# Optimization experiments

Hardware: AMD Instinct MI355X
Metric: run time of the kernel (lower is better)

## Reference

```python
import jax, jax.numpy as jnp
import numpy as np

H, KV, D, EPS = 32, 8, 128, 1e-6
G = H // KV  # kv groups = 4
ROPE_THETA = 5000000.0


def _rms_norm(x, gamma):
    # x: (..., D)
    return x * jax.lax.rsqrt(jnp.mean(x * x, axis=-1, keepdims=True) + EPS) * gamma


def _rotate_half(x):
    x1, x2 = jnp.split(x, 2, axis=-1)
    return jnp.concatenate([-x2, x1], axis=-1)


def _apply_rope(x, cos, sin):
    # x: (b, h, s, D); cos/sin: (b, s, 1, D) -> (b, 1, s, D)
    cos = jnp.transpose(cos, (0, 2, 1, 3))
    sin = jnp.transpose(sin, (0, 2, 1, 3))
    return x * cos + _rotate_half(x) * sin


def setup_inputs() -> dict:
    key = jax.random.key(0)
    ks = jax.random.split(key, 8)
    b, s, hid = 2, 2048, 2560
    hidden = jax.random.normal(ks[0], (b, s, hid), dtype=jnp.float32)
    # realistic RoPE tables (half-split convention matching _rotate_half)
    inv_freq = 1.0 / (ROPE_THETA ** (np.arange(0, D, 2, dtype=np.float32) / D))  # (D/2,)
    pos = np.arange(s, dtype=np.float32)
    freqs = np.outer(pos, inv_freq)                     # (s, D/2)
    emb = np.concatenate([freqs, freqs], axis=-1)       # (s, D)
    cos = jnp.broadcast_to(jnp.asarray(np.cos(emb))[None, :, None, :], (b, s, 1, D))
    sin = jnp.broadcast_to(jnp.asarray(np.sin(emb))[None, :, None, :], (b, s, 1, D))
    sc = 1.0 / np.sqrt(hid)
    wq = jax.random.normal(ks[1], (H * D, hid), dtype=jnp.float32) * sc
    wk = jax.random.normal(ks[2], (KV * D, hid), dtype=jnp.float32) * sc
    wv = jax.random.normal(ks[3], (KV * D, hid), dtype=jnp.float32) * sc
    wo = jax.random.normal(ks[4], (hid, H * D), dtype=jnp.float32) * (1.0 / np.sqrt(H * D))
    q_gamma = jnp.ones((D,), dtype=jnp.float32)
    k_gamma = jnp.ones((D,), dtype=jnp.float32)
    return {"hidden": hidden, "cos": cos, "sin": sin, "wq": wq, "wk": wk,
            "wv": wv, "wo": wo, "q_gamma": q_gamma, "k_gamma": k_gamma}


def reference(hidden, cos, sin, wq, wk, wv, wo, q_gamma, k_gamma):
    b, s, _ = hidden.shape
    # projections -> (b, heads, s, D)
    q = (hidden @ wq.T).reshape(b, s, H, D).transpose(0, 2, 1, 3)
    k = (hidden @ wk.T).reshape(b, s, KV, D).transpose(0, 2, 1, 3)
    v = (hidden @ wv.T).reshape(b, s, KV, D).transpose(0, 2, 1, 3)
    # QK-RMSNorm over head_dim
    q = _rms_norm(q, q_gamma)
    k = _rms_norm(k, k_gamma)
    # RoPE
    q = _apply_rope(q, cos, sin)
    k = _apply_rope(k, cos, sin)
    new_k, new_v = k, v  # kv cache (no prior cache)
    # GQA attention without materializing expanded K/V
    qg = q.reshape(b, KV, G, s, D)
    scale = 1.0 / np.sqrt(D)
    scores = jnp.einsum('bkgqd,bkld->bkgql', qg, k) * scale  # (b,KV,G,s,s)
    causal = jnp.tril(jnp.ones((s, s), dtype=bool))
    scores = jnp.where(causal, scores, jnp.finfo(scores.dtype).min)
    probs = jax.nn.softmax(scores, axis=-1)
    out = jnp.einsum('bkgql,bkld->bkgqd', probs, v)          # (b,KV,G,s,D)
    out = out.reshape(b, H, s, D).transpose(0, 2, 1, 3).reshape(b, s, H * D)
    return (out @ wo.T, new_k, new_v)
```

## Files before the change

kernel.cpp:

```cpp
#include <hip/hip_runtime.h>
#include <stdint.h>

typedef unsigned short u16;
typedef __attribute__((ext_vector_type(8))) short short8;
typedef __attribute__((ext_vector_type(4))) float f32x4;

#define MFMA_BF16(a,b,c) __builtin_amdgcn_mfma_f32_16x16x32_bf16((a),(b),(c),0,0,0)

__device__ __forceinline__ u16 f2bf(float x) {
    uint32_t u = __builtin_bit_cast(uint32_t, x);
    u += 0x7fffu + ((u >> 16) & 1u);
    return (u16)(u >> 16);
}
__device__ __forceinline__ float bf2f(u16 u) {
    return __builtin_bit_cast(float, (uint32_t)u << 16);
}
__device__ __forceinline__ void glds16(const void* g, void* lds) {
    __builtin_amdgcn_global_load_lds((const __attribute__((address_space(1))) void*)g,
                                     (__attribute__((address_space(3))) void*)lds,
                                     16, 0, 0);
}

__device__ __forceinline__ void cvt4(const float* __restrict__ s,
                                     u16* __restrict__ d, int i) {
    float4 v = *(const float4*)(s + i);
    ushort4 o;
    o.x = f2bf(v.x); o.y = f2bf(v.y); o.z = f2bf(v.z); o.w = f2bf(v.w);
    *(ushort4*)(d + i) = o;
}
__global__ __launch_bounds__(256) void cvt_all(
        const float* __restrict__ s0, u16* __restrict__ d0,
        const float* __restrict__ s1, u16* __restrict__ d1,
        const float* __restrict__ s2, u16* __restrict__ d2,
        const float* __restrict__ s3, u16* __restrict__ d3,
        const float* __restrict__ s4, u16* __restrict__ d4)
{
    int i = (blockIdx.x * 256 + threadIdx.x) * 4;
    if      (i < 10485760) cvt4(s0, d0, i);
    else if (i < 20971520) cvt4(s1, d1, i - 10485760);
    else if (i < 23592960) cvt4(s2, d2, i - 20971520);
    else if (i < 26214400) cvt4(s3, d3, i - 23592960);
    else if (i < 36700160) cvt4(s4, d4, i - 26214400);
}

template<bool BF16_OUT>
__global__ __launch_bounds__(256) void gemm_bt(const u16* __restrict__ A,
                                               const u16* __restrict__ B,
                                               void* __restrict__ Cv,
                                               int K, int lda, int ldb, int ldc)
{
    __shared__ __align__(16) u16 As[128 * 64];
    __shared__ __align__(16) u16 Bs[128 * 64];
    const int t = threadIdx.x;
    const int w = t >> 6, l = t & 63;
    const int m0 = blockIdx.y * 128, n0 = blockIdx.x * 128;
    const int wm = (w & 1) * 64, wn = (w >> 1) * 64;
    const int lrow = l & 15, lk = l >> 4;

    f32x4 acc[4][4];
#pragma unroll
    for (int i = 0; i < 4; i++)
#pragma unroll
        for (int j = 0; j < 4; j++) acc[i][j] = (f32x4){0.f, 0.f, 0.f, 0.f};

    const int row_b = w * 8 + (l >> 3);
    const int gsw = ((l & 7) ^ (l >> 3)) * 8;
    const u16* Ap[4]; const u16* Bp[4];
#pragma unroll
    for (int i = 0; i < 4; i++) {
        Ap[i] = A + (size_t)(m0 + row_b + i * 32) * lda + gsw;
        Bp[i] = B + (size_t)(n0 + row_b + i * 32) * ldb + gsw;
    }
    char* Asb = (char*)As + w * 1024;
    char* Bsb = (char*)Bs + w * 1024;

    for (int k0 = 0; k0 < K; k0 += 64) {
        __syncthreads();
#pragma unroll
        for (int i = 0; i < 4; i++) glds16(Ap[i] + k0, Asb + i * 4096);
#pragma unroll
        for (int i = 0; i < 4; i++) glds16(Bp[i] + k0, Bsb + i * 4096);
        __syncthreads();
#pragma unroll
        for (int k2 = 0; k2 < 2; k2++) {
            const int slb = (k2 * 4 + lk) ^ (lrow & 7);
            short8 af[4], bf[4];
#pragma unroll
            for (int mi = 0; mi < 4; mi++)
                af[mi] = *(const short8*)&As[(wm + mi * 16 + lrow) * 64 + slb * 8];
#pragma unroll
            for (int ni = 0; ni < 4; ni++)
                bf[ni] = *(const short8*)&Bs[(wn + ni * 16 + lrow) * 64 + slb * 8];
#pragma unroll
            for (int mi = 0; mi < 4; mi++)
#pragma unroll
                for (int ni = 0; ni < 4; ni++)
                    acc[mi][ni] = MFMA_BF16(af[mi], bf[ni], acc[mi][ni]);
        }
    }

#pragma unroll
    for (int mi = 0; mi < 4; mi++) {
#pragma unroll
        for (int r = 0; r < 4; r++) {
            int row = m0 + wm + mi * 16 + lk * 4 + r;
#pragma unroll
            for (int ni = 0; ni < 4; ni++) {
                int col = n0 + wn + ni * 16 + lrow;
                float v = acc[mi][ni][r];
                if (BF16_OUT) ((u16*)Cv)[(size_t)row * ldc + col] = f2bf(v);
                else          ((float*)Cv)[(size_t)row * ldc + col] = v;
            }
        }
    }
}

__global__ __launch_bounds__(256) void norm_rope_qk(const u16* __restrict__ qkv,
        const float* __restrict__ cosb, const float* __restrict__ sinb,
        const float* __restrict__ qg, const float* __restrict__ kg,
        u16* __restrict__ qb, u16* __restrict__ kb, float* __restrict__ k_out)
{
    const int idx = blockIdx.x * 4 + (threadIdx.x >> 6);
    const int l = threadIdx.x & 63;
    const int tok = idx / 40, hd = idx - tok * 40;
    const int b = tok >> 11, pos = tok & 2047;
    const u16* row = qkv + (size_t)tok * 6144 + hd * 128;
    float x1 = bf2f(row[l]), x2 = bf2f(row[l + 64]);
    float ss = x1 * x1 + x2 * x2;
#pragma unroll
    for (int m = 1; m < 64; m <<= 1) ss += __shfl_xor(ss, m, 64);
    float rn = rsqrtf(ss * (1.0f / 128.0f) + 1e-6f);

    const float* gm = (hd < 32) ? qg : kg;
    float xn1 = x1 * rn * gm[l];
    float xn2 = x2 * rn * gm[l + 64];
    float c1 = cosb[(size_t)tok * 128 + l],      s1 = sinb[(size_t)tok * 128 + l];
    float c2 = cosb[(size_t)tok * 128 + l + 64], s2 = sinb[(size_t)tok * 128 + l + 64];
    float y1 = xn1 * c1 - xn2 * s1;
    float y2 = xn2 * c2 + xn1 * s2;
    if (hd < 32) {
        const float qs = 0.08838834764831845f;
        size_t base = (((size_t)b * 32 + hd) * 2048 + pos) * 128;
        qb[base + l]      = f2bf(y1 * qs);
        qb[base + l + 64] = f2bf(y2 * qs);
    } else {
        int kv = hd - 32;
        size_t base = (((size_t)b * 8 + kv) * 2048 + pos) * 128;
        k_out[base + l] = y1; k_out[base + l + 64] = y2;
        kb[base + l] = f2bf(y1); kb[base + l + 64] = f2bf(y2);
    }
}

__global__ __launch_bounds__(256) void v_pack(const u16* __restrict__ qkv,
        float* __restrict__ v_out, u16* __restrict__ vtb)
{
    __shared__ __align__(16) u16 T[64 * 128];
    const int pb = blockIdx.x, bkv = blockIdx.y;
    const int b = bkv >> 3, kv = bkv & 7;
    const int p0 = pb * 64;
    const int t = threadIdx.x;
    const int pos = t >> 2, ch4 = t & 3;
    const u16* src = qkv + (size_t)(b * 2048 + p0 + pos) * 6144 + (40 + kv) * 128 + ch4 * 32;
    float* vdst = v_out + ((size_t)bkv * 2048 + p0 + pos) * 128 + ch4 * 32;
#pragma unroll
    for (int j = 0; j < 4; j++) {
        short8 x = *(const short8*)(src + j * 8);
        float4 f0, f1;
        f0.x = bf2f(x[0]); f0.y = bf2f(x[1]); f0.z = bf2f(x[2]); f0.w = bf2f(x[3]);
        f1.x = bf2f(x[4]); f1.y = bf2f(x[5]); f1.z = bf2f(x[6]); f1.w = bf2f(x[7]);
        *(float4*)(vdst + j * 8)     = f0;
        *(float4*)(vdst + j * 8 + 4) = f1;
        int slot = (ch4 * 4 + j) ^ (pos & 7);
        *(short8*)&T[pos * 128 + slot * 8] = x;
    }
    __syncthreads();
    const int d = t & 127, ph = t >> 7;
    u16* obase = vtb + ((size_t)bkv * 128 + d) * 2048 + p0 + ph * 32;
#pragma unroll
    for (int g = 0; g < 4; g++) {
        short8 tv;
#pragma unroll
        for (int jj = 0; jj < 8; jj++) {
            int pp = ph * 32 + g * 8 + jj;
            int slot = (d >> 3) ^ (pp & 7);
            tv[jj] = (short)T[pp * 128 + slot * 8 + (d & 7)];
        }
        *(short8*)(obase + g * 8) = tv;
    }
}

__global__ __launch_bounds__(256, 3) void attn_kernel(const u16* __restrict__ qb,
        const u16* __restrict__ kb, const u16* __restrict__ vtb,
        u16* __restrict__ ao)
{
    __shared__ __align__(16) u16 Ks[64 * 128];
    __shared__ __align__(16) u16 Vs[128 * 64];
    __shared__ __align__(16) u16 Ps[4][32 * 72];

    const int bh = blockIdx.x;
    const int b = bh >> 5, h = bh & 31;
    const int kvh = h >> 2;
    const int qt = (int)gridDim.y - 1 - (int)blockIdx.y;
    const int q0 = qt * 128;
    const int t = threadIdx.x, w = t >> 6, l = t & 63;
    const int lrow = l & 15, lk = l >> 4;

    const u16* qbase  = qb  + ((size_t)b * 32 + h)  * 2048 * 128;
    const u16* kbase  = kb  + ((size_t)b * 8 + kvh) * 2048 * 128;
    const u16* vtbase = vtb + ((size_t)b * 8 + kvh) * 128 * 2048;

    short8 qf[2][4];
#pragma unroll
    for (int m = 0; m < 2; m++) {
        const u16* qrow = qbase + (size_t)(q0 + w * 32 + m * 16 + lrow) * 128 + lk * 8;
#pragma unroll
        for (int ks = 0; ks < 4; ks++) qf[m][ks] = *(const short8*)(qrow + ks * 32);
    }

    f32x4 o[2][8];
#pragma unroll
    for (int m = 0; m < 2; m++)
#pragma unroll
        for (int i = 0; i < 8; i++) o[m][i] = (f32x4){0.f, 0.f, 0.f, 0.f};
    float lsum[2][4] = {{0.f,0.f,0.f,0.f},{0.f,0.f,0.f,0.f}};

    int kR[4], kG[4], vR[4], vG[4];
#pragma unroll
    for (int i = 0; i < 4; i++) {
        int c = i * 256 + t;
        kR[i] = c >> 4; kG[i] = (c & 15) ^ (kR[i] & 7);
        vR[i] = c >> 3; vG[i] = (c & 7)  ^ (vR[i] & 7);
    }
    char* Ksb = (char*)Ks + w * 1024;
    char* Vsb = (char*)Vs + w * 1024;
    u16* pw = &Ps[w][0];
    const int wrow_max = q0 + w * 32 + 31;

    const int nkt = 2 * qt + 2;
    for (int kt = 0; kt < nkt; kt++) {
        const int kv0 = kt * 64;
        __syncthreads();
#pragma unroll
        for (int i = 0; i < 4; i++)
            glds16(kbase + (size_t)(kv0 + kR[i]) * 128 + kG[i] * 8, Ksb + i * 4096);
#pragma unroll
        for (int i = 0; i < 4; i++)
            glds16(vtbase + (size_t)vR[i] * 2048 + kv0 + vG[i] * 8, Vsb + i * 4096);
        __syncthreads();

        if (kv0 > wrow_max) continue;

        f32x4 s[2][4];
#pragma unroll
        for (int m = 0; m < 2; m++)
#pragma unroll
            for (int i = 0; i < 4; i++) s[m][i] = (f32x4){0.f, 0.f, 0.f, 0.f};
#pragma unroll
        for (int ks = 0; ks < 4; ks++) {
#pragma unroll
            for (int nt = 0; nt < 4; nt++) {
                int r = nt * 16 + lrow;
                int sl = (ks * 4 + lk) ^ (r & 7);
                short8 kf = *(const short8*)&Ks[r * 128 + sl * 8];
                s[0][nt] = MFMA_BF16(qf[0][ks], kf, s[0][nt]);
                s[1][nt] = MFMA_BF16(qf[1][ks], kf, s[1][nt]);
            }
        }

#pragma unroll
        for (int m = 0; m < 2; m++) {
            const int rowbase = q0 + w * 32 + m * 16;
            if (kv0 + 63 > rowbase) {
#pragma unroll
                for (int nt = 0; nt < 4; nt++) {
                    int cg = kv0 + nt * 16 + lrow;
#pragma unroll
                    for (int r = 0; r < 4; r++)
                        if (cg > rowbase + lk * 4 + r) s[m][nt][r] = -1e30f;
                }
            }
#pragma unroll
            for (int nt = 0; nt < 4; nt++)
#pragma unroll
                for (int r = 0; r < 4; r++) {
                    float p = __expf(s[m][nt][r]);
                    s[m][nt][r] = p;
                    lsum[m][r] += p;
                    pw[(m * 16 + lk * 4 + r) * 72 + nt * 16 + lrow] = f2bf(p);
                }
        }
        asm volatile("s_waitcnt lgkmcnt(0)" ::: "memory");

#pragma unroll
        for (int k2 = 0; k2 < 2; k2++) {
            short8 pf0 = *(const short8*)&pw[lrow * 72 + k2 * 32 + lk * 8];
            short8 pf1 = *(const short8*)&pw[(16 + lrow) * 72 + k2 * 32 + lk * 8];
#pragma unroll
            for (int nt = 0; nt < 8; nt++) {
                int rr = nt * 16 + lrow;
                int sl = (k2 * 4 + lk) ^ (rr & 7);
                short8 vf = *(const short8*)&Vs[rr * 64 + sl * 8];
                o[0][nt] = MFMA_BF16(pf0, vf, o[0][nt]);
                o[1][nt] = MFMA_BF16(pf1, vf, o[1][nt]);
            }
        }
    }

#pragma unroll
    for (int m = 0; m < 2; m++)
#pragma unroll
        for (int r = 0; r < 4; r++) {
            float v = lsum[m][r];
            v += __shfl_xor(v, 1, 64);
            v += __shfl_xor(v, 2, 64);
            v += __shfl_xor(v, 4, 64);
            v += __shfl_xor(v, 8, 64);
            lsum[m][r] = 1.0f / v;
        }
#pragma unroll
    for (int m = 0; m < 2; m++)
#pragma unroll
        for (int nt = 0; nt < 8; nt++)
#pragma unroll
            for (int r = 0; r < 4; r++) {
                int tok = q0 + w * 32 + m * 16 + lk * 4 + r;
                size_t off = ((size_t)b * 2048 + tok) * 4096 + h * 128 + nt * 16 + lrow;
                ao[off] = f2bf(o[m][nt][r] * lsum[m][r]);
            }
}

extern "C" void kernel_launch(void* const* d_in, const int* in_sizes, int n_in,
                              void* d_out, int out_size, void* d_ws, size_t ws_size,
                              hipStream_t stream)
{
    (void)in_sizes; (void)n_in; (void)out_size; (void)ws_size;
    const float* hidden = (const float*)d_in[0];
    const float* cosb   = (const float*)d_in[1];
    const float* sinb   = (const float*)d_in[2];
    const float* wq     = (const float*)d_in[3];
    const float* wk     = (const float*)d_in[4];
    const float* wv     = (const float*)d_in[5];
    const float* wo     = (const float*)d_in[6];
    const float* qg     = (const float*)d_in[7];
    const float* kg     = (const float*)d_in[8];

    float* out   = (float*)d_out;
    float* k_out = out + (size_t)2 * 2048 * 2560;
    float* v_out = k_out + (size_t)2 * 8 * 2048 * 128;

    u16* hid_b = (u16*)d_ws;
    u16* w_b   = hid_b + 10485760;
    u16* wo_b  = w_b   + 15728640;
    u16* q_b   = wo_b  + 10485760;
    u16* k_b   = q_b   + 16777216;
    u16* vt_b  = k_b   + 4194304;
    u16* qkv_b = vt_b  + 4194304;
    u16* ao_b  = hid_b;

    cvt_all<<<35840, 256, 0, stream>>>(hidden, hid_b, wq, w_b,
                                       wk, w_b + 10485760, wv, w_b + 13107200,
                                       wo, wo_b);

    gemm_bt<true><<<dim3(48, 32), 256, 0, stream>>>(hid_b, w_b, qkv_b,
                                                    2560, 2560, 2560, 6144);
    norm_rope_qk<<<40960, 256, 0, stream>>>(qkv_b, cosb, sinb, qg, kg,
                                            q_b, k_b, k_out);
    v_pack<<<dim3(32, 16), 256, 0, stream>>>(qkv_b, v_out, vt_b);
    attn_kernel<<<dim3(64, 16), 256, 0, stream>>>(q_b, k_b, vt_b, ao_b);
    gemm_bt<false><<<dim3(20, 32), 256, 0, stream>>>(ao_b, wo_b, out,
                                                     4096, 4096, 4096, 2560);
}
```

Baseline: 676.8 us.

## Replace GEMM with 256x256 8-wave double-buffered pipelined kernel

After: 603.9 us. -10.8%, faster.

```diff
diff --git a/kernel.cpp b/kernel.cpp
--- a/kernel.cpp
+++ b/kernel.cpp
@@ -6,6 +6,10 @@
 typedef __attribute__((ext_vector_type(4))) float f32x4;
 
 #define MFMA_BF16(a,b,c) __builtin_amdgcn_mfma_f32_16x16x32_bf16((a),(b),(c),0,0,0)
+
+#define S_BARRIER()  asm volatile("s_barrier" ::: "memory")
+#define WAIT_LGKM0() asm volatile("s_waitcnt lgkmcnt(0)" ::: "memory")
+#define WAIT_VM(N)   asm volatile("s_waitcnt vmcnt(" #N ")" ::: "memory")
 
 __device__ __forceinline__ u16 f2bf(float x) {
     uint32_t u = __builtin_bit_cast(uint32_t, x);
@@ -43,71 +47,144 @@
     else if (i < 36700160) cvt4(s4, d4, i - 26214400);
 }
 
+template<int MH, int NH>
+__device__ __forceinline__ void mm16(f32x4 (&acc)[8][4],
+                                     const short8 (&a)[4][2],
+                                     const short8 (&b)[2][2]) {
+#pragma unroll
+    for (int k2 = 0; k2 < 2; k2++)
+#pragma unroll
+        for (int mi = 0; mi < 4; mi++)
+#pragma unroll
+            for (int nj = 0; nj < 2; nj++)
+                acc[MH * 4 + mi][NH * 2 + nj] =
+                    MFMA_BF16(a[mi][k2], b[nj][k2], acc[MH * 4 + mi][NH * 2 + nj]);
+}
+
 template<bool BF16_OUT>
-__global__ __launch_bounds__(256) void gemm_bt(const u16* __restrict__ A,
-                                               const u16* __restrict__ B,
-                                               void* __restrict__ Cv,
-                                               int K, int lda, int ldb, int ldc)
-{
-    __shared__ __align__(16) u16 As[128 * 64];
-    __shared__ __align__(16) u16 Bs[128 * 64];
+__global__ __launch_bounds__(512, 2) void gemm8(const u16* __restrict__ A,
+                                                const u16* __restrict__ B,
+                                                void* __restrict__ Cv,
+                                                int K, int lda, int ldb, int ldc,
+                                                int ntn)
+{
+    __shared__ __align__(16) u16 Sm[65536];
     const int t = threadIdx.x;
     const int w = t >> 6, l = t & 63;
-    const int m0 = blockIdx.y * 128, n0 = blockIdx.x * 128;
-    const int wm = (w & 1) * 64, wn = (w >> 1) * 64;
     const int lrow = l & 15, lk = l >> 4;
-
-    f32x4 acc[4][4];
-#pragma unroll
-    for (int i = 0; i < 4; i++)
+    const int wm = w >> 2, wn = w & 3;
+
+    const int nwg = (int)gridDim.x;
+    const int cpx = nwg >> 3;
+    const int id = (int)blockIdx.x;
+    const int sw = (id & 7) * cpx + (id >> 3);
+    const int tm = sw / ntn, tn = sw - tm * ntn;
+    const int m0 = tm * 256, n0 = tn * 256;
+
+    const int nkt = K >> 6;
+    const size_t laneOffA = (size_t)(w * 16 + (l >> 3)) * lda + (((l & 7) ^ (l >> 3)) * 8);
+    const size_t laneOffB = (size_t)(w * 16 + (l >> 3)) * ldb + (((l & 7) ^ (l >> 3)) * 8);
+    const u16* Ag = A + (size_t)m0 * lda;
+    const u16* Bg = B + (size_t)n0 * ldb;
+
+    auto STAGE_A = [&](int kt, int slot, int h) {
+#pragma unroll
+        for (int j = 0; j < 2; j++)
+            glds16(Ag + laneOffA + (size_t)(h * 128 + j * 8) * lda + kt * 64,
+                   (char*)Sm + slot * 65536 + h * 16384 + w * 2048 + j * 1024);
+    };
+    auto STAGE_B = [&](int kt, int slot, int h) {
+#pragma unroll
+        for (int j = 0; j < 2; j++)
+            glds16(Bg + laneOffB + (size_t)(h * 128 + j * 8) * ldb + kt * 64,
+                   (char*)Sm + 32768 + slot * 65536 + h * 16384 + w * 2048 + j * 1024);
+    };
+    auto READ_A = [&](short8 (&a)[4][2], int slot, int rb) {
+#pragma unroll
+        for (int mi = 0; mi < 4; mi++)
+#pragma unroll
+            for (int k2 = 0; k2 < 2; k2++) {
+                int row = rb + mi * 16 + lrow;
+                a[mi][k2] = *(const short8*)&Sm[slot * 32768 + row * 64 +
+                                                (((k2 * 4 + lk) ^ (lrow & 7)) * 8)];
+            }
+    };
+    auto READ_B = [&](short8 (&b)[2][2], int slot, int rb) {
+#pragma unroll
+        for (int nj = 0; nj < 2; nj++)
+#pragma unroll
+            for (int k2 = 0; k2 < 2; k2++) {
+                int row = rb + nj * 16 + lrow;
+                b[nj][k2] = *(const short8*)&Sm[slot * 32768 + 16384 + row * 64 +
+                                                (((k2 * 4 + lk) ^ (lrow & 7)) * 8)];
+            }
+    };
+
+    f32x4 acc[8][4];
+#pragma unroll
+    for (int i = 0; i < 8; i++)
 #pragma unroll
         for (int j = 0; j < 4; j++) acc[i][j] = (f32x4){0.f, 0.f, 0.f, 0.f};
-
-    const int row_b = w * 8 + (l >> 3);
-    const int gsw = ((l & 7) ^ (l >> 3)) * 8;
-    const u16* Ap[4]; const u16* Bp[4];
-#pragma unroll
-    for (int i = 0; i < 4; i++) {
-        Ap[i] = A + (size_t)(m0 + row_b + i * 32) * lda + gsw;
-        Bp[i] = B + (size_t)(n0 + row_b + i * 32) * ldb + gsw;
-    }
-    char* Asb = (char*)As + w * 1024;
-    char* Bsb = (char*)Bs + w * 1024;
-
-    for (int k0 = 0; k0 < K; k0 += 64) {
-        __syncthreads();
-#pragma unroll
-        for (int i = 0; i < 4; i++) glds16(Ap[i] + k0, Asb + i * 4096);
-#pragma unroll
-        for (int i = 0; i < 4; i++) glds16(Bp[i] + k0, Bsb + i * 4096);
-        __syncthreads();
-#pragma unroll
-        for (int k2 = 0; k2 < 2; k2++) {
-            const int slb = (k2 * 4 + lk) ^ (lrow & 7);
-            short8 af[4], bf[4];
-#pragma unroll
-            for (int mi = 0; mi < 4; mi++)
-                af[mi] = *(const short8*)&As[(wm + mi * 16 + lrow) * 64 + slb * 8];
-#pragma unroll
-            for (int ni = 0; ni < 4; ni++)
-                bf[ni] = *(const short8*)&Bs[(wn + ni * 16 + lrow) * 64 + slb * 8];
-#pragma unroll
-            for (int mi = 0; mi < 4; mi++)
-#pragma unroll
-                for (int ni = 0; ni < 4; ni++)
-                    acc[mi][ni] = MFMA_BF16(af[mi], bf[ni], acc[mi][ni]);
-        }
-    }
-
-#pragma unroll
-    for (int mi = 0; mi < 4; mi++) {
+    short8 aF0[4][2], aF1[4][2], bF0[2][2], bF1[2][2];
+
+    STAGE_A(0, 0, 0); STAGE_A(0, 0, 1);
+    STAGE_B(0, 0, 0); STAGE_B(0, 0, 1);
+    const int k1 = (nkt > 1) ? 1 : 0;
+    STAGE_A(k1, 1, 0); STAGE_A(k1, 1, 1);
+    WAIT_VM(4);
+    S_BARRIER();
+
+    for (int kt = 0; kt < nkt; ++kt) {
+        const int slot = kt & 1, nslot = slot ^ 1;
+        const int ktB = (kt + 1 < nkt) ? kt + 1 : kt;
+        const int ktA = (kt + 2 < nkt) ? kt + 2 : kt;
+        READ_A(aF0, slot, wm * 128);
+        READ_B(bF0, slot, wn * 64);
+        STAGE_B(ktB, nslot, 0);
+        S_BARRIER();
+        WAIT_LGKM0();
+        __builtin_amdgcn_sched_barrier(0);
+        __builtin_amdgcn_s_setprio(1);
+        mm16<0, 0>(acc, aF0, bF0);
+        __builtin_amdgcn_s_setprio(0);
+        S_BARRIER();
+        READ_A(aF1, slot, wm * 128 + 64);
+        STAGE_B(ktB, nslot, 1);
+        S_BARRIER();
+        WAIT_LGKM0();
+        __builtin_amdgcn_sched_barrier(0);
+        __builtin_amdgcn_s_setprio(1);
+        mm16<1, 0>(acc, aF1, bF0);
+        __builtin_amdgcn_s_setprio(0);
+        S_BARRIER();
+        READ_B(bF1, slot, wn * 64 + 32);
+        STAGE_A(ktA, slot, 0);
+        S_BARRIER();
+        WAIT_LGKM0();
+        __builtin_amdgcn_sched_barrier(0);
+        __builtin_amdgcn_s_setprio(1);
+        mm16<1, 1>(acc, aF1, bF1);
+        __builtin_amdgcn_s_setprio(0);
+        S_BARRIER();
+        STAGE_A(ktA, slot, 1);
+        S_BARRIER();
+        __builtin_amdgcn_s_setprio(1);
+        mm16<0, 1>(acc, aF0, bF1);
+        __builtin_amdgcn_s_setprio(0);
+        WAIT_VM(4);
+        S_BARRIER();
+    }
+    WAIT_VM(0);
+
+#pragma unroll
+    for (int mi = 0; mi < 8; mi++) {
 #pragma unroll
         for (int r = 0; r < 4; r++) {
-            int row = m0 + wm + mi * 16 + lk * 4 + r;
-#pragma unroll
-            for (int ni = 0; ni < 4; ni++) {
-                int col = n0 + wn + ni * 16 + lrow;
-                float v = acc[mi][ni][r];
+            int row = m0 + wm * 128 + mi * 16 + lk * 4 + r;
+#pragma unroll
+            for (int nj = 0; nj < 4; nj++) {
+                int col = n0 + wn * 64 + nj * 16 + lrow;
+                float v = acc[mi][nj][r];
                 if (BF16_OUT) ((u16*)Cv)[(size_t)row * ldc + col] = f2bf(v);
                 else          ((float*)Cv)[(size_t)row * ldc + col] = v;
             }
@@ -361,12 +438,12 @@
                                        wk, w_b + 10485760, wv, w_b + 13107200,
                                        wo, wo_b);
 
-    gemm_bt<true><<<dim3(48, 32), 256, 0, stream>>>(hid_b, w_b, qkv_b,
-                                                    2560, 2560, 2560, 6144);
+    gemm8<true><<<dim3(384), 512, 0, stream>>>(hid_b, w_b, qkv_b,
+                                               2560, 2560, 2560, 6144, 24);
     norm_rope_qk<<<40960, 256, 0, stream>>>(qkv_b, cosb, sinb, qg, kg,
                                             q_b, k_b, k_out);
     v_pack<<<dim3(32, 16), 256, 0, stream>>>(qkv_b, v_out, vt_b);
     attn_kernel<<<dim3(64, 16), 256, 0, stream>>>(q_b, k_b, vt_b, ao_b);
-    gemm_bt<false><<<dim3(20, 32), 256, 0, stream>>>(ao_b, wo_b, out,
-                                                     4096, 4096, 4096, 2560);
-}
+    gemm8<false><<<dim3(160), 512, 0, stream>>>(ao_b, wo_b, out,
+                                                4096, 4096, 4096, 2560, 10);
+}
```
